# Kernel tuning notes

Measured on AMD Instinct MI355X. Metric: run time of the kernel, lower is better.

The kernel has to match this reference:

```python
import jax, jax.numpy as jnp
import numpy as np

N = 65536      # flattened tokens
K = 8192       # codebook_size
D = 64         # codebook_dim
DECAY = 0.9
EPS = 1e-05


def setup_inputs() -> dict:
    key = jax.random.key(0)
    k1, k2, k3, k4 = jax.random.split(key, 4)
    z = jax.random.normal(k1, (N, D), dtype=jnp.float32)
    # codebook initialized uniform(-1, 1) in the torch module
    weight = jax.random.uniform(k2, (K, D), dtype=jnp.float32, minval=-1.0, maxval=1.0)
    # EMA state: positive cluster sizes, embed_avg near the codebook
    cluster_size = jax.random.uniform(k3, (K,), dtype=jnp.float32)
    embed_avg = weight + 0.01 * jax.random.normal(k4, (K, D), dtype=jnp.float32)
    return {"z": z, "weight": weight, "cluster_size": cluster_size, "embed_avg": embed_avg}


def reference(z, weight, cluster_size, embed_avg):
    # VectorQuantizer.ema_update: distances -> argmin -> gather -> EMA stats -> weight refresh
    zd = jax.lax.stop_gradient(z)  # torch uses z.detach() for distance/quant_error
    # distance[n,k] = ||z_n||^2 + ||c_k||^2 - 2 z_n . c_k   (addmm pattern)
    dist = (zd * zd).sum(1, keepdims=True) + (weight * weight).sum(1) - 2.0 * (zd @ weight.T)  # [N, K]
    token = jnp.argmin(dist, axis=1)                      # [N]
    embed = weight[token]                                  # gather [N, D]
    quant_error = jnp.mean(((embed - zd) ** 2).sum(1))

    # onehot_probs.sum(0) == per-code counts; onehot.T @ z == segment sum of z
    counts = jax.ops.segment_sum(jnp.ones((zd.shape[0],), zd.dtype), token, num_segments=K)  # [K]
    embed_sum = jax.ops.segment_sum(z, token, num_segments=K)                                # [K, D]

    new_cluster_size = cluster_size * DECAY + (1.0 - DECAY) * counts
    new_embed_avg = embed_avg * DECAY + (1.0 - DECAY) * embed_sum

    # ema_weight_update with num_tokens = codebook_size
    n = new_cluster_size.sum()
    smoothed = (new_cluster_size + EPS) / (n + K * EPS) * n
    new_weight = new_embed_avg / smoothed[:, None]

    return quant_error, new_weight, new_cluster_size, new_embed_avg
```

## Files before the change

kernel.cpp:

```cpp
#include <hip/hip_runtime.h>
#include <type_traits>

#define N_TOK 65536
#define K_CODE 8192
#define D_DIM 64

constexpr float DECAY = 0.9f;
constexpr float OMD = 0.1f;
constexpr float EPS = 1e-5f;

constexpr int OUT_QE = 0;
constexpr int OUT_W  = 1;
constexpr int OUT_CS = 1 + K_CODE * D_DIM;
constexpr int OUT_EA = OUT_CS + K_CODE;

constexpr int WS_QE     = 0;
constexpr int WS_NSUM   = 1;
constexpr int WS_COUNTS = 16;
constexpr int WS_EMBSUM = WS_COUNTS + K_CODE;
constexpr int WS_WHI    = WS_EMBSUM + K_CODE * D_DIM;
constexpr int WS_WLO    = WS_WHI + K_CODE * D_DIM / 2;
constexpr int WS_CNP    = WS_WLO + K_CODE * D_DIM / 2;
constexpr int WS_ZERO   = WS_WHI;

typedef __attribute__((ext_vector_type(16))) float floatx16;
typedef __attribute__((ext_vector_type(8)))  short short8;
typedef __attribute__((ext_vector_type(8)))  __bf16 bf16x8;

template <typename T, typename = void> struct mfma_takes : std::false_type {};
template <typename T>
struct mfma_takes<T, std::void_t<decltype(__builtin_amdgcn_mfma_f32_32x32x16_bf16(
    std::declval<T>(), std::declval<T>(), std::declval<floatx16>(), 0, 0, 0))>>
    : std::true_type {};

__device__ __forceinline__ floatx16 MFMA(short8 a, short8 b, floatx16 c) {
  if constexpr (mfma_takes<bf16x8>::value) {
    return __builtin_amdgcn_mfma_f32_32x32x16_bf16(
        __builtin_bit_cast(bf16x8, a), __builtin_bit_cast(bf16x8, b), c, 0, 0, 0);
  } else {
    return __builtin_amdgcn_mfma_f32_32x32x16_bf16(a, b, c, 0, 0, 0);
  }
}

__device__ __forceinline__ unsigned short bf16rne(float x) {
  unsigned int u = __float_as_uint(x);
  return (unsigned short)((u + 0x7FFFu + ((u >> 16) & 1u)) >> 16);
}

__device__ __forceinline__ void gload_lds16(const unsigned short* g, unsigned short* l) {
#if defined(__has_builtin) && __has_builtin(__builtin_amdgcn_global_load_lds)
  typedef __attribute__((address_space(1))) void gvoid;
  typedef __attribute__((address_space(3))) void lvoid;
  __builtin_amdgcn_global_load_lds((gvoid*)g, (lvoid*)l, 16, 0, 0);
#else
  *(uint4*)l = *(const uint4*)g;
#endif
}

__global__ void vq_prep(const float* __restrict__ w, float* __restrict__ ws) {
  const int tid = threadIdx.x;
  const int d = tid & 63;
  const int k = blockIdx.x * 4 + (tid >> 6);
  const float v = w[(size_t)k * D_DIM + d];
  const unsigned short h = bf16rne(v);
  const float hf = __uint_as_float((unsigned int)h << 16);
  const unsigned short l = bf16rne(v - hf);
  unsigned short* whi = (unsigned short*)(ws + WS_WHI);
  unsigned short* wlo = (unsigned short*)(ws + WS_WLO);
  const int pos = k * D_DIM + (((d >> 3) ^ (k & 7)) * 8) + (d & 7);
  whi[pos] = h;
  wlo[pos] = l;
  float s = v * v;
#pragma unroll
  for (int m = 32; m >= 1; m >>= 1) s += __shfl_xor(s, m);
  if (d == 0) {
    const float cn64 = s + 64.0f;
    const unsigned short ch = bf16rne(cn64);
    const float chf = __uint_as_float((unsigned int)ch << 16);
    const unsigned short cl = bf16rne(cn64 - chf);
    ((unsigned int*)(ws + WS_CNP))[k] = (unsigned int)ch | ((unsigned int)cl << 16);
  }
}

__global__ __launch_bounds__(512, 4) void vq_argmin(
    const float* __restrict__ z, float* __restrict__ ws)
{
  __shared__ __align__(16) unsigned short Wbuf[2][2][2][32 * 64];
  __shared__ float mind_s[2][128];
  __shared__ int   tok_s[2][128];

  const int tid  = threadIdx.x;
  const int w    = tid >> 6;
  const int lane = tid & 63;
  const int m    = lane & 31;
  const int h    = lane >> 5;
  const int tg   = w & 3;
  const int hw   = w >> 2;
  const int tb   = blockIdx.x * 128;

  const unsigned short* whi = (const unsigned short*)(ws + WS_WHI);
  const unsigned short* wlo = (const unsigned short*)(ws + WS_WLO);
  const unsigned int*   cnp = (const unsigned int*)(ws + WS_CNP);

  short8 ah[4], al[4];
  float znorm = 0.f;
  {
    const float* zrow = z + (size_t)(tb + tg * 32 + m) * D_DIM + 8 * h;
#pragma unroll
    for (int s4 = 0; s4 < 4; ++s4) {
      const float4 v0 = *(const float4*)(zrow + 16 * s4);
      const float4 v1 = *(const float4*)(zrow + 16 * s4 + 4);
      const float vals[8] = {v0.x, v0.y, v0.z, v0.w, v1.x, v1.y, v1.z, v1.w};
#pragma unroll
      for (int j = 0; j < 8; ++j) {
        const float x = vals[j];
        znorm += x * x;
        const float y = -2.0f * x;
        const unsigned short hb = bf16rne(y);
        const float hf = __uint_as_float((unsigned int)hb << 16);
        const unsigned short lb = bf16rne(y - hf);
        ah[s4][j] = (short)hb;
        al[s4][j] = (short)lb;
      }
    }
    znorm += __shfl_xor(znorm, 32);
  }

  short8 acn;
  {
    uint4 ab = {0u, 0u, 0u, 0u};
    ab.x = (h == 0) ? 0x3F803F80u : 0u;
    acn = __builtin_bit_cast(short8, ab);
  }

  float kmin[16];
#pragma unroll
  for (int r = 0; r < 16; ++r) kmin[r] = 3.4e38f;

  auto issueStage = [&](int s, int b) {
#pragma unroll
    for (int i = 0; i < 2; ++i) {
      const int t = w * 2 + i;
      const int half = t >> 3, plane = (t >> 2) & 1, seg = t & 3;
      const unsigned short* src = (plane ? wlo : whi)
          + ((size_t)half * 4096 + (size_t)s * 32) * D_DIM + seg * 512 + lane * 8;
      unsigned short* dst = &Wbuf[half][b][plane][seg * 512];
      gload_lds16(src, dst);
    }
  };

  int xoff[4];
#pragma unroll
  for (int s4 = 0; s4 < 4; ++s4) xoff[s4] = ((2 * s4 + h) ^ (m & 7)) * 8;
  const int mrow = m * 64;

  issueStage(0, 0);
  __syncthreads();

  const floatx16 kZero = {};

  for (int s = 0; s < 128; ++s) {
    const int b = s & 1;
    const unsigned int cnq = cnp[hw * 4096 + s * 32 + m];
    if (s + 1 < 128) issueStage(s + 1, b ^ 1);

    short8 bh[4], bl[4];
#pragma unroll
    for (int s4 = 0; s4 < 4; ++s4) {
      bh[s4] = *(const short8*)&Wbuf[hw][b][0][mrow + xoff[s4]];
      bl[s4] = *(const short8*)&Wbuf[hw][b][1][mrow + xoff[s4]];
    }
    short8 bcn;
    {
      uint4 bb = {0u, 0u, 0u, 0u};
      bb.x = (h == 0) ? cnq : 0u;
      bcn = __builtin_bit_cast(short8, bb);
    }

    floatx16 acc = MFMA(acn, bcn, kZero);
#pragma unroll
    for (int s4 = 0; s4 < 4; ++s4) acc = MFMA(ah[s4], bh[s4], acc);
#pragma unroll
    for (int s4 = 0; s4 < 4; ++s4) acc = MFMA(al[s4], bh[s4], acc);
#pragma unroll
    for (int s4 = 0; s4 < 4; ++s4) acc = MFMA(ah[s4], bl[s4], acc);

#pragma unroll
    for (int r = 0; r < 16; ++r) {
      kmin[r] = fminf(kmin[r],
          __uint_as_float((__float_as_uint(acc[r]) & 0xFFFFFF00u) | (unsigned)s));
    }
    __syncthreads();
  }

#pragma unroll
  for (int r = 0; r < 16; ++r) {
    float kv = kmin[r];
    int mo = m;
#pragma unroll
    for (int mm = 1; mm < 32; mm <<= 1) {
      const float ov = __shfl_xor(kv, mm);
      const int   om = __shfl_xor(mo, mm);
      if (ov < kv || (ov == kv && om < mo)) { kv = ov; mo = om; }
    }
    const int mr = (r & 3) + 8 * (r >> 2) + 4 * h;
    if (m == mr) {
      const unsigned int kb = __float_as_uint(kv);
      tok_s[hw][tg * 32 + mr] = hw * 4096 + (int)(kb & 0xFFu) * 32 + mo;
      mind_s[hw][tg * 32 + mr] =
          __uint_as_float(kb & 0xFFFFFF00u) - 64.0f + znorm;
    }
  }
  __syncthreads();

  float* counts = ws + WS_COUNTS;
  float* embsum = ws + WS_EMBSUM;

  if (tid < 128) {
    const float d0 = mind_s[0][tid], d1 = mind_s[1][tid];
    const int   i0 = tok_s[0][tid],  i1 = tok_s[1][tid];
    const bool t1 = d1 < d0;
    const float dm = t1 ? d1 : d0;
    const int   im = t1 ? i1 : i0;
    tok_s[0][tid] = im;
    float qe = dm;
#pragma unroll
    for (int mm = 32; mm >= 1; mm >>= 1) qe += __shfl_xor(qe, mm);
    if ((tid & 63) == 0) atomicAdd(ws + WS_QE, qe);
    atomicAdd(&counts[im], 1.0f);
  }
  __syncthreads();

#pragma unroll 4
  for (int t = 0; t < 16; ++t) {
    const int row = w * 16 + t;
    const int tk = tok_s[0][row];
    const float zv = z[(size_t)(tb + row) * D_DIM + lane];
    atomicAdd(&embsum[(size_t)tk * D_DIM + lane], zv);
  }
}

__global__ void vq_finalize_cs(const float* __restrict__ cluster_size,
                               float* __restrict__ ws, float* __restrict__ out)
{
  const int k = blockIdx.x * 256 + threadIdx.x;
  const float ncs = cluster_size[k] * DECAY + OMD * ws[WS_COUNTS + k];
  out[OUT_CS + k] = ncs;
  float s = ncs;
#pragma unroll
  for (int m = 32; m >= 1; m >>= 1) s += __shfl_xor(s, m);
  __shared__ float part[4];
  if ((threadIdx.x & 63) == 0) part[threadIdx.x >> 6] = s;
  __syncthreads();
  if (threadIdx.x == 0) {
    atomicAdd(ws + WS_NSUM, part[0] + part[1] + part[2] + part[3]);
    if (blockIdx.x == 0) out[OUT_QE] = ws[WS_QE] * (1.0f / N_TOK);
  }
}

__global__ void vq_finalize_w(const float* __restrict__ embed_avg,
                              const float* __restrict__ ws, float* __restrict__ out)
{
  const int idx = blockIdx.x * 256 + threadIdx.x;
  const int k = idx >> 6;
  const float nea = embed_avg[idx] * DECAY + OMD * ws[WS_EMBSUM + idx];
  out[OUT_EA + idx] = nea;
  const float n = ws[WS_NSUM];
  const float ncs = out[OUT_CS + k];
  const float sm = (ncs + EPS) / (n + K_CODE * EPS) * n;
  out[OUT_W + idx] = nea / sm;
}

extern "C" void kernel_launch(void* const* d_in, const int* in_sizes, int n_in,
                              void* d_out, int out_size, void* d_ws, size_t ws_size,
                              hipStream_t stream) {
  const float* z  = (const float*)d_in[0];
  const float* w  = (const float*)d_in[1];
  const float* cs = (const float*)d_in[2];
  const float* ea = (const float*)d_in[3];
  float* out = (float*)d_out;
  float* ws  = (float*)d_ws;

  (void)hipMemsetAsync(d_ws, 0, (size_t)WS_ZERO * sizeof(float), stream);

  vq_prep<<<K_CODE / 4, 256, 0, stream>>>(w, ws);
  vq_argmin<<<N_TOK / 128, 512, 0, stream>>>(z, ws);
  vq_finalize_cs<<<K_CODE / 256, 256, 0, stream>>>(cs, ws, out);
  vq_finalize_w<<<K_CODE * D_DIM / 256, 256, 0, stream>>>(ea, ws, out);
}
```

Before: 290.2 us.

## Deepen codebook LDS pipeline to four buffers and merge finalize kernels

```diff
diff --git a/kernel.cpp b/kernel.cpp
--- a/kernel.cpp
+++ b/kernel.cpp
@@ -57,7 +57,8 @@
 #endif
 }
 
-__global__ void vq_prep(const float* __restrict__ w, float* __restrict__ ws) {
+__global__ void vq_prep(const float* __restrict__ w, const float* __restrict__ cs,
+                        float* __restrict__ ws) {
   const int tid = threadIdx.x;
   const int d = tid & 63;
   const int k = blockIdx.x * 4 + (tid >> 6);
@@ -79,13 +80,14 @@
     const float chf = __uint_as_float((unsigned int)ch << 16);
     const unsigned short cl = bf16rne(cn64 - chf);
     ((unsigned int*)(ws + WS_CNP))[k] = (unsigned int)ch | ((unsigned int)cl << 16);
+    atomicAdd(ws + WS_NSUM + (k & 7), DECAY * cs[k]);
   }
 }
 
 __global__ __launch_bounds__(512, 4) void vq_argmin(
     const float* __restrict__ z, float* __restrict__ ws)
 {
-  __shared__ __align__(16) unsigned short Wbuf[2][2][2][32 * 64];
+  __shared__ __align__(16) unsigned short Wbuf[2][4][2][32 * 64];
   __shared__ float mind_s[2][128];
   __shared__ int   tok_s[2][128];
 
@@ -137,14 +139,14 @@
 #pragma unroll
   for (int r = 0; r < 16; ++r) kmin[r] = 3.4e38f;
 
-  auto issueStage = [&](int s, int b) {
+  auto issueStage = [&](int sIdx, int bufIdx) {
 #pragma unroll
     for (int i = 0; i < 2; ++i) {
       const int t = w * 2 + i;
       const int half = t >> 3, plane = (t >> 2) & 1, seg = t & 3;
       const unsigned short* src = (plane ? wlo : whi)
-          + ((size_t)half * 4096 + (size_t)s * 32) * D_DIM + seg * 512 + lane * 8;
-      unsigned short* dst = &Wbuf[half][b][plane][seg * 512];
+          + ((size_t)half * 4096 + (size_t)sIdx * 32) * D_DIM + seg * 512 + lane * 8;
+      unsigned short* dst = &Wbuf[half][bufIdx][plane][seg * 512];
       gload_lds16(src, dst);
     }
   };
@@ -155,14 +157,19 @@
   const int mrow = m * 64;
 
   issueStage(0, 0);
-  __syncthreads();
+  issueStage(1, 1);
+  unsigned int cnq_cur = cnp[hw * 4096 + m];
 
   const floatx16 kZero = {};
 
   for (int s = 0; s < 128; ++s) {
-    const int b = s & 1;
-    const unsigned int cnq = cnp[hw * 4096 + s * 32 + m];
-    if (s + 1 < 128) issueStage(s + 1, b ^ 1);
+    const int b = s & 3;
+    const unsigned int cnq_next = cnp[hw * 4096 + ((s + 1) & 127) * 32 + m];
+    issueStage((s + 2) & 127, (s + 2) & 3);
+
+    asm volatile("s_waitcnt vmcnt(6)" ::: "memory");
+    __builtin_amdgcn_s_barrier();
+    asm volatile("" ::: "memory");
 
     short8 bh[4], bl[4];
 #pragma unroll
@@ -173,10 +180,11 @@
     short8 bcn;
     {
       uint4 bb = {0u, 0u, 0u, 0u};
-      bb.x = (h == 0) ? cnq : 0u;
+      bb.x = (h == 0) ? cnq_cur : 0u;
       bcn = __builtin_bit_cast(short8, bb);
     }
 
+    __builtin_amdgcn_s_setprio(1);
     floatx16 acc = MFMA(acn, bcn, kZero);
 #pragma unroll
     for (int s4 = 0; s4 < 4; ++s4) acc = MFMA(ah[s4], bh[s4], acc);
@@ -184,13 +192,14 @@
     for (int s4 = 0; s4 < 4; ++s4) acc = MFMA(al[s4], bh[s4], acc);
 #pragma unroll
     for (int s4 = 0; s4 < 4; ++s4) acc = MFMA(ah[s4], bl[s4], acc);
+    __builtin_amdgcn_s_setprio(0);
 
 #pragma unroll
     for (int r = 0; r < 16; ++r) {
       kmin[r] = fminf(kmin[r],
           __uint_as_float((__float_as_uint(acc[r]) & 0xFFFFFF00u) | (unsigned)s));
     }
-    __syncthreads();
+    cnq_cur = cnq_next;
   }
 
 #pragma unroll
@@ -240,35 +249,22 @@
   }
 }
 
-__global__ void vq_finalize_cs(const float* __restrict__ cluster_size,
-                               float* __restrict__ ws, float* __restrict__ out)
-{
-  const int k = blockIdx.x * 256 + threadIdx.x;
-  const float ncs = cluster_size[k] * DECAY + OMD * ws[WS_COUNTS + k];
-  out[OUT_CS + k] = ncs;
-  float s = ncs;
-#pragma unroll
-  for (int m = 32; m >= 1; m >>= 1) s += __shfl_xor(s, m);
-  __shared__ float part[4];
-  if ((threadIdx.x & 63) == 0) part[threadIdx.x >> 6] = s;
-  __syncthreads();
-  if (threadIdx.x == 0) {
-    atomicAdd(ws + WS_NSUM, part[0] + part[1] + part[2] + part[3]);
-    if (blockIdx.x == 0) out[OUT_QE] = ws[WS_QE] * (1.0f / N_TOK);
-  }
-}
-
-__global__ void vq_finalize_w(const float* __restrict__ embed_avg,
-                              const float* __restrict__ ws, float* __restrict__ out)
+__global__ void vq_finalize(const float* __restrict__ cluster_size,
+                            const float* __restrict__ embed_avg,
+                            const float* __restrict__ ws, float* __restrict__ out)
 {
   const int idx = blockIdx.x * 256 + threadIdx.x;
   const int k = idx >> 6;
+  const float ncs = cluster_size[k] * DECAY + OMD * ws[WS_COUNTS + k];
   const float nea = embed_avg[idx] * DECAY + OMD * ws[WS_EMBSUM + idx];
   out[OUT_EA + idx] = nea;
-  const float n = ws[WS_NSUM];
-  const float ncs = out[OUT_CS + k];
+  float n = OMD * (float)N_TOK;
+#pragma unroll
+  for (int i = 0; i < 8; ++i) n += ws[WS_NSUM + i];
   const float sm = (ncs + EPS) / (n + K_CODE * EPS) * n;
   out[OUT_W + idx] = nea / sm;
+  if ((idx & 63) == 0) out[OUT_CS + k] = ncs;
+  if (idx == 0) out[OUT_QE] = ws[WS_QE] * (1.0f / N_TOK);
 }
 
 extern "C" void kernel_launch(void* const* d_in, const int* in_sizes, int n_in,
@@ -283,8 +279,7 @@
 
   (void)hipMemsetAsync(d_ws, 0, (size_t)WS_ZERO * sizeof(float), stream);
 
-  vq_prep<<<K_CODE / 4, 256, 0, stream>>>(w, ws);
+  vq_prep<<<K_CODE / 4, 256, 0, stream>>>(w, cs, ws);
   vq_argmin<<<N_TOK / 128, 512, 0, stream>>>(z, ws);
-  vq_finalize_cs<<<K_CODE / 256, 256, 0, stream>>>(cs, ws, out);
-  vq_finalize_w<<<K_CODE * D_DIM / 256, 256, 0, stream>>>(ea, ws, out);
-}
+  vq_finalize<<<K_CODE * D_DIM / 256, 256, 0, stream>>>(cs, ea, ws, out);
+}
```

Result: slower. 384.7 us (+32.6%).
